# Kernel optimization log

Measured on AMD Instinct MI355X. Metric: run time of the kernel, lower is better.

The kernel has to match this reference:

```python
import jax, jax.numpy as jnp
import numpy as np

P = 7  # pool_size (module fast path: pool_size=7, C=512)


def setup_inputs() -> dict:
    key = jax.random.key(0)
    B, N, H, W, C = 2, 64, 38, 38, 512
    k1, k2, k3, k4, k5 = jax.random.split(key, 5)
    feature_map = jax.random.normal(k1, (B, H, W, C), dtype=jnp.float32)
    # ROI = (y, x, h, w) in integer feature-map coordinates, h,w >= P so every
    # pooling cell is non-empty and the bin boundaries partition the ROI exactly
    # (the original's max(size,1) clamp is then a no-op).
    h = jax.random.randint(k2, (B, N), P, H + 1, dtype=jnp.int32)
    w = jax.random.randint(k3, (B, N), P, W + 1, dtype=jnp.int32)
    y = jnp.floor(jax.random.uniform(k4, (B, N)) * (H - h + 1).astype(jnp.float32)).astype(jnp.int32)
    x = jnp.floor(jax.random.uniform(k5, (B, N)) * (W - w + 1).astype(jnp.float32)).astype(jnp.int32)
    rois = jnp.stack([y, x, h, w], axis=-1)
    return {"feature_map": feature_map, "rois": rois}


def _roi_pool(feature_map, rois, pool_size=P):
    # feature_map: [B,H,W,C] float, rois: [B,N,4] int (y, x, h, w)
    B, H, W, C = feature_map.shape
    N = rois.shape[1]
    PP = pool_size * pool_size
    y0 = rois[..., 0][:, :, None]  # [B,N,1]
    x0 = rois[..., 1][:, :, None]
    h = rois[..., 2][:, :, None]
    w = rois[..., 3][:, :, None]

    # For a pixel at relative row r inside an ROI of height h (h >= pool_size),
    # its bin b is the largest b with floor(b*h/pool_size) <= r, i.e.
    # b = (pool_size*r + pool_size-1) // h  -- identical to the original's
    # [floor(b*h/P), floor((b+1)*h/P)) partition (last bin end = h).
    rel_y = jnp.arange(H, dtype=jnp.int32)[None, None, :] - y0  # [B,N,H]
    rel_x = jnp.arange(W, dtype=jnp.int32)[None, None, :] - x0  # [B,N,W]
    ybin = (pool_size * rel_y + (pool_size - 1)) // jnp.maximum(h, 1)
    xbin = (pool_size * rel_x + (pool_size - 1)) // jnp.maximum(w, 1)
    valid_y = (rel_y >= 0) & (rel_y < h)  # [B,N,H]
    valid_x = (rel_x >= 0) & (rel_x < w)  # [B,N,W]

    cell = ybin[:, :, :, None] * pool_size + xbin[:, :, None, :]  # [B,N,H,W]
    valid = valid_y[:, :, :, None] & valid_x[:, :, None, :]
    cell = jnp.where(valid, cell, PP)  # PP = dump cell for out-of-ROI pixels

    roi_id = jnp.arange(B * N, dtype=jnp.int32).reshape(B, N, 1, 1)
    seg = (roi_id * (PP + 1) + cell).reshape(-1)  # [B*N*H*W]

    # Values: feature map broadcast over the ROI axis -> one fused segment-max.
    vals = jnp.broadcast_to(feature_map[:, None], (B, N, H, W, C)).reshape(-1, C)
    pooled = jax.ops.segment_max(vals, seg, num_segments=B * N * (PP + 1))
    pooled = pooled.reshape(B, N, PP + 1, C)[:, :, :PP]  # drop dump cell
    return pooled.reshape(B, N, pool_size, pool_size, C)


def reference(feature_map, rois):
    return _roi_pool(feature_map, rois)
```

## Files before the change

### kernel.cpp

```cpp
#include <hip/hip_runtime.h>
#include <hip/hip_bf16.h>
#include <math.h>

#define RB 2
#define RN 64
#define RH 38
#define RW 38
#define RC 512
#define RP 7

__global__ __launch_bounds__(128) void roi_pool_kernel(
    const float* __restrict__ fm, const int* __restrict__ rois,
    float* __restrict__ out) {
  int cell = blockIdx.x;
  int px = cell % RP;
  int t = cell / RP;
  int py = t % RP;
  t /= RP;
  int n = t % RN;
  int b = t / RN;

  const int* r = rois + ((b * RN + n) << 2);
  int y0 = r[0], x0 = r[1], h = r[2], w = r[3];

  int ys = (py * h) / RP, ye = ((py + 1) * h) / RP;
  int xs = (px * w) / RP, xe = ((px + 1) * w) / RP;

  int tid = threadIdx.x;
  int cbase = tid << 2;

  float4 m = make_float4(-INFINITY, -INFINITY, -INFINITY, -INFINITY);

  for (int yy = ys; yy < ye; ++yy) {
    const float* rowp =
        fm + ((size_t)((b * RH + y0 + yy) * RW + x0 + xs)) * RC + cbase;
    for (int xx = xs; xx < xe; ++xx) {
      float4 v = *(const float4*)rowp;
      m.x = fmaxf(m.x, v.x);
      m.y = fmaxf(m.y, v.y);
      m.z = fmaxf(m.z, v.z);
      m.w = fmaxf(m.w, v.w);
      rowp += RC;
    }
  }

  *(float4*)(out + (size_t)cell * RC + cbase) = m;
}

extern "C" void kernel_launch(void* const* d_in, const int* in_sizes, int n_in,
                              void* d_out, int out_size, void* d_ws, size_t ws_size,
                              hipStream_t stream) {
  const float* fm = (const float*)d_in[0];
  const int* rois = (const int*)d_in[1];
  float* out = (float*)d_out;

  int n_cells = RB * RN * RP * RP;
  roi_pool_kernel<<<n_cells, 128, 0, stream>>>(fm, rois, out);
}
```

Before: 74.95 us.

## Map two pool cells per block, flatten bin loop with prefetch, nontemporal stores

Each 128-thread block now handles two adjacent pooling cells, one per wavefront, with each lane covering eight channels through two float4 loads. The block index is remapped so neighbouring blocks are spread across the two images, which may change cache or channel locality. The nested row/column loop is flattened into one loop with a one-step software prefetch and pointer-wrap arithmetic. Outputs are written with nontemporal stores to avoid polluting cache. This halves the block count and adds memory-level parallelism per thread, at the cost of more registers.

```diff
diff --git a/kernel.cpp b/kernel.cpp
--- a/kernel.cpp
+++ b/kernel.cpp
@@ -8,43 +8,73 @@
 #define RW 38
 #define RC 512
 #define RP 7
+#define CELLS (RB * RN * RP * RP)
+#define CPI (RN * RP * RP)
+#define PPI (CPI / 2)
+
+typedef float vfloat4 __attribute__((ext_vector_type(4)));
 
 __global__ __launch_bounds__(128) void roi_pool_kernel(
     const float* __restrict__ fm, const int* __restrict__ rois,
     float* __restrict__ out) {
-  int cell = blockIdx.x;
+  int wave = threadIdx.x >> 6;
+  int lane = threadIdx.x & 63;
+
+  int bx = blockIdx.x;
+  int x = bx & 7;
+  int j = bx >> 3;
+  int img = x >> 2;
+  int pair = img * PPI + ((j << 2) | (x & 3));
+  int cell = pair * 2 + wave;
+
   int px = cell % RP;
   int t = cell / RP;
   int py = t % RP;
   t /= RP;
-  int n = t % RN;
   int b = t / RN;
 
-  const int* r = rois + ((b * RN + n) << 2);
+  const int* r = rois + (t << 2);
   int y0 = r[0], x0 = r[1], h = r[2], w = r[3];
 
   int ys = (py * h) / RP, ye = ((py + 1) * h) / RP;
   int xs = (px * w) / RP, xe = ((px + 1) * w) / RP;
+  int bw = xe - xs;
+  int cnt = bw * (ye - ys);
 
-  int tid = threadIdx.x;
-  int cbase = tid << 2;
+  const float4* p =
+      (const float4*)(fm +
+                      (size_t)((b * RH + y0 + ys) * RW + x0 + xs) * RC) +
+      lane;
+  const int pixstep = RC / 4;
+  const int wrapstep = (RW - bw) * (RC / 4);
 
-  float4 m = make_float4(-INFINITY, -INFINITY, -INFINITY, -INFINITY);
+  float4 m0 = make_float4(-INFINITY, -INFINITY, -INFINITY, -INFINITY);
+  float4 m1 = m0;
 
-  for (int yy = ys; yy < ye; ++yy) {
-    const float* rowp =
-        fm + ((size_t)((b * RH + y0 + yy) * RW + x0 + xs)) * RC + cbase;
-    for (int xx = xs; xx < xe; ++xx) {
-      float4 v = *(const float4*)rowp;
-      m.x = fmaxf(m.x, v.x);
-      m.y = fmaxf(m.y, v.y);
-      m.z = fmaxf(m.z, v.z);
-      m.w = fmaxf(m.w, v.w);
-      rowp += RC;
-    }
+  float4 a0 = p[0];
+  float4 a1 = p[64];
+  int xrem = bw;
+  for (int k = 1; k < cnt; ++k) {
+    p += pixstep;
+    if (--xrem == 0) { xrem = bw; p += wrapstep; }
+    float4 n0 = p[0];
+    float4 n1 = p[64];
+    m0.x = fmaxf(m0.x, a0.x); m0.y = fmaxf(m0.y, a0.y);
+    m0.z = fmaxf(m0.z, a0.z); m0.w = fmaxf(m0.w, a0.w);
+    m1.x = fmaxf(m1.x, a1.x); m1.y = fmaxf(m1.y, a1.y);
+    m1.z = fmaxf(m1.z, a1.z); m1.w = fmaxf(m1.w, a1.w);
+    a0 = n0; a1 = n1;
   }
+  m0.x = fmaxf(m0.x, a0.x); m0.y = fmaxf(m0.y, a0.y);
+  m0.z = fmaxf(m0.z, a0.z); m0.w = fmaxf(m0.w, a0.w);
+  m1.x = fmaxf(m1.x, a1.x); m1.y = fmaxf(m1.y, a1.y);
+  m1.z = fmaxf(m1.z, a1.z); m1.w = fmaxf(m1.w, a1.w);
 
-  *(float4*)(out + (size_t)cell * RC + cbase) = m;
+  vfloat4* o = (vfloat4*)(out + (size_t)cell * RC) + lane;
+  vfloat4 s0 = {m0.x, m0.y, m0.z, m0.w};
+  vfloat4 s1 = {m1.x, m1.y, m1.z, m1.w};
+  __builtin_nontemporal_store(s0, o);
+  __builtin_nontemporal_store(s1, o + 64);
 }
 
 extern "C" void kernel_launch(void* const* d_in, const int* in_sizes, int n_in,
@@ -54,6 +84,5 @@
   const int* rois = (const int*)d_in[1];
   float* out = (float*)d_out;
 
-  int n_cells = RB * RN * RP * RP;
-  roi_pool_kernel<<<n_cells, 128, 0, stream>>>(fm, rois, out);
+  roi_pool_kernel<<<CELLS / 2, 128, 0, stream>>>(fm, rois, out);
 }
```

Measured after the change: 69.55 us. 7.2% less time.
